# Kernel optimization log

Hardware: AMD Instinct MI355X
Metric: run time of the kernel (lower is better)

## Reference

```python
import jax, jax.numpy as jnp
import numpy as np

TOP_K = 4  # num_experts_per_tok


def setup_inputs() -> dict:
    key = jax.random.key(0)
    ks = jax.random.split(key, 5)
    T, H, M, E = 2048, 1024, 512, 32
    sH = 1.0 / np.sqrt(H)
    sM = 1.0 / np.sqrt(M)
    return {
        "x": jax.random.normal(ks[0], (T, 1, H), dtype=jnp.float32),
        "gate_w": jax.random.normal(ks[1], (E, H), dtype=jnp.float32) * sH,   # router nn.Linear weight [E, H]
        "w_gate": jax.random.normal(ks[2], (E, M, H), dtype=jnp.float32) * sH,  # ffn_gate_exps, per expert [M, H]
        "w_up": jax.random.normal(ks[3], (E, M, H), dtype=jnp.float32) * sH,    # ffn_up_exps
        "w_down": jax.random.normal(ks[4], (E, H, M), dtype=jnp.float32) * sM,  # ffn_down_exps, per expert [H, M]
    }


def reference(x, gate_w, w_gate, w_up, w_down):
    # x: [T, S, H]; only the last position is used (decode path)
    curr = x[:, -1, :]                                   # [T, H]
    T = curr.shape[0]
    E = gate_w.shape[0]

    # router: logits = curr @ gate_w^T, top-k, softmax over top-k logits
    logits = curr @ gate_w.T                             # [T, E]
    topk_vals, topk_ids = jax.lax.top_k(logits, TOP_K)   # [T, K]
    topk_weights = jax.nn.softmax(topk_vals, axis=-1)    # [T, K]

    # dense routing matrix [T, E]: weight for chosen experts, 0 elsewhere
    route = jnp.zeros((T, E), dtype=curr.dtype)
    route = route.at[jnp.arange(T)[:, None], topk_ids].add(topk_weights)

    # expert MLPs: gate/up -> silu(gate)*up -> down, weighted combine
    gate_act = jnp.einsum('th,emh->tem', curr, w_gate)   # [T, E, M]
    up_act = jnp.einsum('th,emh->tem', curr, w_up)
    mixed = jax.nn.silu(gate_act) * up_act * route[:, :, None]
    out = jnp.einsum('tem,ehm->th', mixed, w_down)       # [T, H]

    return out.reshape(T, 1, -1)
```

## Files before the change

kernel.cpp:

```cpp
#include <hip/hip_runtime.h>
#include <math.h>

#define T_TOK 2048
#define H_DIM 1024
#define M_DIM 512
#define E_NUM 32
#define TOPK  4

#define MAXT  63
#define SLOTS (MAXT * 256)

typedef __bf16 bf16x8 __attribute__((ext_vector_type(8)));
typedef float f32x4 __attribute__((ext_vector_type(4)));
typedef unsigned short u16x8 __attribute__((ext_vector_type(8)));
typedef unsigned short u16x4 __attribute__((ext_vector_type(4)));

__device__ __forceinline__ unsigned short f2bf(float f) {
  unsigned u = __float_as_uint(f);
  return (unsigned short)((u + 0x7fffu + ((u >> 16) & 1u)) >> 16);
}
__device__ __forceinline__ f32x4 mfma16(bf16x8 a, bf16x8 b, f32x4 c) {
  return __builtin_amdgcn_mfma_f32_16x16x32_bf16(a, b, c, 0, 0, 0);
}
__device__ __forceinline__ void gload16(const void* g, void* l) {
  __builtin_amdgcn_global_load_lds(
      (const __attribute__((address_space(1))) unsigned int*)g,
      (__attribute__((address_space(3))) unsigned int*)l, 16, 0, 0);
}

__global__ __launch_bounds__(256) void gating_kernel(
    const float* __restrict__ x, const float* __restrict__ gate_w,
    unsigned short* __restrict__ xh,
    float* __restrict__ topk_w, int* __restrict__ cursors,
    int* __restrict__ tok_list) {
  __shared__ float xr[H_DIM];
  __shared__ float logits[E_NUM];
  int t = blockIdx.x;
  int tid = threadIdx.x;
  const float* xrow = x + (size_t)t * H_DIM;
  float4 v = *(const float4*)(xrow + tid * 4);
  *(float4*)(xr + tid * 4) = v;
  {
    float f[4] = {v.x, v.y, v.z, v.w};
    u16x4 hv;
    #pragma unroll
    for (int j = 0; j < 4; ++j) hv[j] = f2bf(f[j]);
    *(u16x4*)(xh + (size_t)t * H_DIM + tid * 4) = hv;
  }
  __syncthreads();
  int wave = tid >> 6, lane = tid & 63;
  const float4* x4 = (const float4*)xr;
  for (int e8 = 0; e8 < 8; ++e8) {
    int e = wave * 8 + e8;
    const float4* g4 = (const float4*)(gate_w + (size_t)e * H_DIM);
    float p = 0.f;
    #pragma unroll
    for (int i = 0; i < 4; ++i) {
      float4 a = x4[lane + i * 64];
      float4 b = g4[lane + i * 64];
      p += a.x * b.x + a.y * b.y + a.z * b.z + a.w * b.w;
    }
    for (int off = 32; off > 0; off >>= 1) p += __shfl_down(p, off, 64);
    if (lane == 0) logits[e] = p;
  }
  __syncthreads();
  if (tid == 0) {
    float vv[E_NUM];
    for (int e = 0; e < E_NUM; ++e) vv[e] = logits[e];
    int ids[TOPK]; float vals[TOPK];
    for (int k = 0; k < TOPK; ++k) {
      int bi = 0; float bv = -1e30f;
      for (int e = 0; e < E_NUM; ++e) if (vv[e] > bv) { bv = vv[e]; bi = e; }
      ids[k] = bi; vals[k] = bv; vv[bi] = -1e30f;
    }
    float m = vals[0];
    float w[TOPK]; float s = 0.f;
    for (int k = 0; k < TOPK; ++k) { w[k] = expf(vals[k] - m); s += w[k]; }
    float inv = 1.f / s;
    for (int k = 0; k < TOPK; ++k) {
      int g = t * TOPK + k;
      topk_w[g] = w[k] * inv;
      int slot = atomicAdd(&cursors[ids[k]], 1);
      tok_list[ids[k] * T_TOK + slot] = g;
    }
  }
}

__global__ void build_tiles(const int* __restrict__ cursors,
                            int* __restrict__ n_tiles, int* __restrict__ tile_info) {
  int lane = threadIdx.x;
  int c = (lane < E_NUM) ? cursors[lane] : 0;
  int nt = (c + 255) >> 8;
  int pfx = nt;
  for (int off = 1; off < 64; off <<= 1) {
    int v = __shfl_up(pfx, off, 64);
    if (lane >= off) pfx += v;
  }
  if (lane == E_NUM - 1) n_tiles[0] = pfx;
  int excl = pfx - nt;
  if (lane < E_NUM)
    for (int i = 0; i < nt; ++i) tile_info[excl + i] = (lane << 8) | i;
}

__global__ __launch_bounds__(256) void fill_slots(
    const int* __restrict__ cursors, const int* __restrict__ n_tiles,
    const int* __restrict__ tile_info, const int* __restrict__ tok_list,
    int* __restrict__ slot_pair) {
  int b = blockIdx.x;
  int tid = threadIdx.x;
  int pair = -1;
  if (b < n_tiles[0]) {
    int info = tile_info[b];
    int e = info >> 8, i = info & 255;
    int idx = i * 256 + tid;
    if (idx < cursors[e]) pair = tok_list[e * T_TOK + idx];
  }
  slot_pair[b * 256 + tid] = pair;
}

template <int MODE>
__global__ __launch_bounds__(512, 2) void gemm256(
    const unsigned short* __restrict__ xh,
    const unsigned short* __restrict__ mixed,
    const float* __restrict__ w_gate, const float* __restrict__ w_up,
    const float* __restrict__ w_down,
    const int* __restrict__ n_tiles, const int* __restrict__ tile_info,
    const int* __restrict__ slot_pair,
    unsigned short* __restrict__ gu_raw, float* __restrict__ out) {
  constexpr int KT = (MODE == 0) ? H_DIM : M_DIM;
  constexpr int NKS = KT / 64;
  int tidx = blockIdx.y;
  if (tidx >= n_tiles[0]) return;
  int info = tile_info[tidx];
  int e = info >> 8;
  int n0 = blockIdx.x * 256;
  int slot0 = tidx * 256;
  int tid = threadIdx.x;
  int lane = tid & 63, wid = tid >> 6;

  __shared__ unsigned short L[2][32768];
  __shared__ int sp[256];

  if (tid < 256) sp[tid] = slot_pair[slot0 + tid];
  __syncthreads();

  const unsigned short* asrc[4];
  #pragma unroll
  for (int i = 0; i < 4; ++i) {
    int row = wid * 32 + i * 8 + (lane >> 3);
    int oct = (lane & 7) ^ (row & 7);
    if (MODE == 0) {
      int pr = sp[row];
      int tok = (pr >= 0) ? (pr >> 2) : 0;
      asrc[i] = xh + (size_t)tok * H_DIM + oct * 8;
    } else {
      asrc[i] = mixed + (size_t)(slot0 + row) * M_DIM + oct * 8;
    }
  }

  int brow = tid >> 1, bkh = (tid & 1) * 32;
  const float* bsrc;
  if (MODE == 0) {
    int n = n0 + brow;
    bsrc = (n < M_DIM ? w_gate + ((size_t)e * M_DIM + n) * H_DIM
                      : w_up + ((size_t)e * M_DIM + (n - M_DIM)) * H_DIM) + bkh;
  } else {
    bsrc = w_down + ((size_t)e * H_DIM + n0 + brow) * M_DIM + bkh;
  }
  int bwo[4];
  #pragma unroll
  for (int i = 0; i < 4; ++i)
    bwo[i] = 16384 + brow * 64 + ((((tid & 1) * 4 + i)) ^ (brow & 7)) * 8;

  int wm = wid >> 2, wn = wid & 3;
  f32x4 acc[8][4] = {};
  float fb[32];

#define G_LOADB(K0) { _Pragma("unroll") \
    for (int q = 0; q < 8; ++q) \
      *(float4*)(fb + q * 4) = *(const float4*)(bsrc + (K0) + q * 4); }

#define G_WRITEB(BB) { _Pragma("unroll") \
    for (int i = 0; i < 4; ++i) { \
      bf16x8 v; \
      _Pragma("unroll") \
      for (int j = 0; j < 8; ++j) v[j] = (__bf16)fb[i * 8 + j]; \
      *(bf16x8*)&L[BB][bwo[i]] = v; } }

#define G_DMA_A(BB, K0) { _Pragma("unroll") \
    for (int i = 0; i < 4; ++i) \
      gload16(asrc[i] + (K0), &L[BB][(wid * 32 + i * 8) * 64]); }

#define G_COMPUTE(BB) { _Pragma("unroll") \
    for (int kf = 0; kf < 2; ++kf) { \
      int kl = kf * 4 + (lane >> 4); \
      bf16x8 av[8], bv[4]; \
      _Pragma("unroll") \
      for (int mf = 0; mf < 8; ++mf) { \
        int ra = wm * 128 + mf * 16 + (lane & 15); \
        av[mf] = *(const bf16x8*)&L[BB][ra * 64 + (kl ^ (ra & 7)) * 8]; } \
      _Pragma("unroll") \
      for (int nf = 0; nf < 4; ++nf) { \
        int cb = wn * 64 + nf * 16 + (lane & 15); \
        bv[nf] = *(const bf16x8*)&L[BB][16384 + cb * 64 + (kl ^ (cb & 7)) * 8]; } \
      _Pragma("unroll") \
      for (int mf = 0; mf < 8; ++mf) \
        _Pragma("unroll") \
        for (int nf = 0; nf < 4; ++nf) \
          acc[mf][nf] = mfma16(av[mf], bv[nf], acc[mf][nf]); } }

  G_LOADB(0);
  G_DMA_A(0, 0);
  asm volatile("s_waitcnt vmcnt(0)" ::: "memory");
  __syncthreads();
  G_WRITEB(0);
  G_LOADB(64);

  for (int t = 0; t < NKS; ++t) {
    const int cur = t & 1;
    asm volatile("s_waitcnt vmcnt(0)" ::: "memory");
    __syncthreads();
    if (t + 1 < NKS) {
      G_WRITEB(cur ^ 1);
      G_DMA_A(cur ^ 1, (t + 1) * 64);
    }
    if (t + 2 < NKS) G_LOADB((t + 2) * 64);
    G_COMPUTE(cur);
  }

  if (MODE == 0) {
    #pragma unroll
    for (int mf = 0; mf < 8; ++mf)
      #pragma unroll
      for (int j = 0; j < 4; ++j) {
        int row = wm * 128 + mf * 16 + (lane >> 4) * 4 + j;
        size_t rb = (size_t)(slot0 + row) * 1024 + n0 + wn * 64 + (lane & 15);
        #pragma unroll
        for (int nf = 0; nf < 4; ++nf) {
          __bf16 v = (__bf16)acc[mf][nf][j];
          gu_raw[rb + nf * 16] = *(unsigned short*)&v;
        }
      }
  } else {
    #pragma unroll
    for (int mf = 0; mf < 8; ++mf)
      #pragma unroll
      for (int j = 0; j < 4; ++j) {
        int row = wm * 128 + mf * 16 + (lane >> 4) * 4 + j;
        int pr = sp[row];
        if (pr < 0) continue;
        size_t ob = (size_t)(pr >> 2) * H_DIM + n0 + wn * 64 + (lane & 15);
        #pragma unroll
        for (int nf = 0; nf < 4; ++nf)
          atomicAdd(&out[ob + nf * 16], acc[mf][nf][j]);
      }
  }
}

__global__ __launch_bounds__(256) void silu_kernel(
    const unsigned short* __restrict__ gu, const int* __restrict__ slot_pair,
    const float* __restrict__ topk_w, unsigned short* __restrict__ mixed) {
  int tid = threadIdx.x;
  int slot = blockIdx.x * 4 + (tid >> 6);
  int col = (tid & 63) * 8;
  int pr = slot_pair[slot];
  if (pr < 0) return;
  float w = topk_w[pr];
  const unsigned short* gp = gu + (size_t)slot * 1024 + col;
  u16x8 gg = *(const u16x8*)gp;
  u16x8 uu = *(const u16x8*)(gp + 512);
  bf16x8 o;
  #pragma unroll
  for (int j = 0; j < 8; ++j) {
    float g = __uint_as_float(((unsigned)gg[j]) << 16);
    float u = __uint_as_float(((unsigned)uu[j]) << 16);
    float v = (g / (1.f + __expf(-g))) * u * w;
    o[j] = (__bf16)v;
  }
  *(bf16x8*)(mixed + (size_t)slot * 512 + col) = o;
}

extern "C" void kernel_launch(void* const* d_in, const int* in_sizes, int n_in,
                              void* d_out, int out_size, void* d_ws, size_t ws_size,
                              hipStream_t stream) {
  const float* x      = (const float*)d_in[0];
  const float* gate_w = (const float*)d_in[1];
  const float* w_gate = (const float*)d_in[2];
  const float* w_up   = (const float*)d_in[3];
  const float* w_down = (const float*)d_in[4];
  float* out = (float*)d_out;

  char* ws = (char*)d_ws;
  size_t off = 0;
  float* topk_w    = (float*)(ws + off); off += (size_t)T_TOK * TOPK * 4;
  int*   cursors   = (int*)(ws + off);   off += 256;
  int*   n_tiles   = (int*)(ws + off);   off += 64;
  int*   tile_info = (int*)(ws + off);   off += MAXT * 4 + 64;
  int*   slot_pair = (int*)(ws + off);   off += (size_t)SLOTS * 4;
  int*   tok_list  = (int*)(ws + off);   off += (size_t)E_NUM * T_TOK * 4;
  unsigned short* x_hi   = (unsigned short*)(ws + off); off += (size_t)T_TOK * H_DIM * 2;
  unsigned short* gu_raw = (unsigned short*)(ws + off); off += (size_t)SLOTS * 1024 * 2;
  unsigned short* mixed  = (unsigned short*)(ws + off); off += (size_t)SLOTS * 512 * 2;

  hipMemsetAsync(cursors, 0, E_NUM * sizeof(int), stream);
  hipMemsetAsync(out, 0, (size_t)T_TOK * H_DIM * sizeof(float), stream);

  gating_kernel<<<T_TOK, 256, 0, stream>>>(x, gate_w, x_hi, topk_w,
                                           cursors, tok_list);
  build_tiles<<<1, 64, 0, stream>>>(cursors, n_tiles, tile_info);
  fill_slots<<<MAXT, 256, 0, stream>>>(cursors, n_tiles, tile_info, tok_list,
                                       slot_pair);
  gemm256<0><<<dim3(4, MAXT), 512, 0, stream>>>(
      x_hi, mixed, w_gate, w_up, w_down, n_tiles, tile_info, slot_pair,
      gu_raw, out);
  silu_kernel<<<SLOTS / 4, 256, 0, stream>>>(gu_raw, slot_pair, topk_w, mixed);
  gemm256<1><<<dim3(4, MAXT), 512, 0, stream>>>(
      x_hi, mixed, w_gate, w_up, w_down, n_tiles, tile_info, slot_pair,
      gu_raw, out);
}
```

Baseline: 201.0 us.

## Stream fp32 weights into LDS via direct DMA with triple-buffered K=32 pipeline

The grouped GEMM kernel no longer loads fp32 weight tiles into registers and converts them to bf16 before writing to LDS. Both A (bf16 activations) and B (raw fp32 weights) now go straight to LDS through global_load_lds, and the fp32-to-bf16 conversion happens at fragment read time. The K step drops from 64 to 32, and a three-stage ring buffer with counted vmcnt waits keeps two stages in flight. This aims to hide global latency and free registers, at the cost of more conversion ALU work per MFMA, twice the LDS bytes for B, and twice as many barriers per K.

```diff
diff --git a/kernel.cpp b/kernel.cpp
--- a/kernel.cpp
+++ b/kernel.cpp
@@ -26,6 +26,12 @@
   __builtin_amdgcn_global_load_lds(
       (const __attribute__((address_space(1))) unsigned int*)g,
       (__attribute__((address_space(3))) unsigned int*)l, 16, 0, 0);
+}
+__device__ __forceinline__ bf16x8 cvt8(f32x4 a, f32x4 b) {
+  bf16x8 r;
+  #pragma unroll
+  for (int j = 0; j < 4; ++j) { r[j] = (__bf16)a[j]; r[4 + j] = (__bf16)b[j]; }
+  return r;
 }
 
 __global__ __launch_bounds__(256) void gating_kernel(
@@ -128,7 +134,7 @@
     const int* __restrict__ slot_pair,
     unsigned short* __restrict__ gu_raw, float* __restrict__ out) {
   constexpr int KT = (MODE == 0) ? H_DIM : M_DIM;
-  constexpr int NKS = KT / 64;
+  constexpr int NKS = KT / 32;
   int tidx = blockIdx.y;
   if (tidx >= n_tiles[0]) return;
   int info = tile_info[tidx];
@@ -138,94 +144,102 @@
   int tid = threadIdx.x;
   int lane = tid & 63, wid = tid >> 6;
 
-  __shared__ unsigned short L[2][32768];
+  __shared__ unsigned short L[3][24576];
   __shared__ int sp[256];
 
   if (tid < 256) sp[tid] = slot_pair[slot0 + tid];
   __syncthreads();
 
-  const unsigned short* asrc[4];
-  #pragma unroll
-  for (int i = 0; i < 4; ++i) {
-    int row = wid * 32 + i * 8 + (lane >> 3);
-    int oct = (lane & 7) ^ (row & 7);
-    if (MODE == 0) {
-      int pr = sp[row];
-      int tok = (pr >= 0) ? (pr >> 2) : 0;
-      asrc[i] = xh + (size_t)tok * H_DIM + oct * 8;
+  const unsigned short* asrc0;
+  const unsigned short* asrc1;
+  {
+    #pragma unroll
+    for (int i = 0; i < 2; ++i) {
+      int blk = wid * 2 + i;
+      int row = blk * 16 + (lane >> 2);
+      int oct = ((lane & 3) - ((lane >> 2) >> 1)) & 3;
+      const unsigned short* s;
+      if (MODE == 0) {
+        int pr = sp[row];
+        int tok = (pr >= 0) ? (pr >> 2) : 0;
+        s = xh + (size_t)tok * H_DIM + oct * 8;
+      } else {
+        s = mixed + (size_t)(slot0 + row) * M_DIM + oct * 8;
+      }
+      if (i == 0) asrc0 = s; else asrc1 = s;
+    }
+  }
+  const float* bsrc0; const float* bsrc1; const float* bsrc2; const float* bsrc3;
+  {
+    #pragma unroll
+    for (int i = 0; i < 4; ++i) {
+      int ci = wid * 4 + i;
+      int blk = ci >> 1;
+      int w7 = ((ci & 1) << 6) + lane;
+      int col = blk * 16 + (w7 >> 3);
+      int q = ((w7 & 7) - ((w7 >> 3) & 7)) & 7;
+      const float* base;
+      if (MODE == 0) {
+        int n = n0 + col;
+        base = (n < M_DIM) ? w_gate + ((size_t)e * M_DIM + n) * H_DIM
+                           : w_up + ((size_t)e * M_DIM + (n - M_DIM)) * H_DIM;
+      } else {
+        base = w_down + ((size_t)e * H_DIM + n0 + col) * M_DIM;
+      }
+      base += q * 4;
+      if (i == 0) bsrc0 = base; else if (i == 1) bsrc1 = base;
+      else if (i == 2) bsrc2 = base; else bsrc3 = base;
+    }
+  }
+
+  int wm = wid >> 2, wn = wid & 3;
+  int l15 = lane & 15, o4 = lane >> 4, l7 = lane & 7;
+  f32x4 acc[8][4] = {};
+
+#define STAGE(P, KS) { \
+    gload16(asrc0 + (KS) * 32, &L[P][(wid * 2 + 0) * 512]); \
+    gload16(asrc1 + (KS) * 32, &L[P][(wid * 2 + 1) * 512]); \
+    gload16(bsrc0 + (KS) * 32, &L[P][8192 + (wid * 4 + 0) * 512]); \
+    gload16(bsrc1 + (KS) * 32, &L[P][8192 + (wid * 4 + 1) * 512]); \
+    gload16(bsrc2 + (KS) * 32, &L[P][8192 + (wid * 4 + 2) * 512]); \
+    gload16(bsrc3 + (KS) * 32, &L[P][8192 + (wid * 4 + 3) * 512]); }
+
+#define COMPUTE(P) { \
+    const unsigned short* Ab = &L[P][0]; \
+    const float* Bb = (const float*)&L[P][8192]; \
+    bf16x8 av[8]; bf16x8 bv[4]; \
+    _Pragma("unroll") \
+    for (int mf = 0; mf < 8; ++mf) { \
+      int idx = (wm * 8 + mf) * 512 + l15 * 32 + ((o4 + (l15 >> 1)) & 3) * 8; \
+      av[mf] = *(const bf16x8*)&Ab[idx]; } \
+    _Pragma("unroll") \
+    for (int nf = 0; nf < 4; ++nf) { \
+      int b0 = (wn * 4 + nf) * 512 + l15 * 32 + ((2 * o4 + l7) & 7) * 4; \
+      int b1 = (wn * 4 + nf) * 512 + l15 * 32 + ((2 * o4 + 1 + l7) & 7) * 4; \
+      bv[nf] = cvt8(*(const f32x4*)&Bb[b0], *(const f32x4*)&Bb[b1]); } \
+    _Pragma("unroll") \
+    for (int mf = 0; mf < 8; ++mf) \
+      _Pragma("unroll") \
+      for (int nf = 0; nf < 4; ++nf) \
+        acc[mf][nf] = mfma16(av[mf], bv[nf], acc[mf][nf]); }
+
+  STAGE(0, 0);
+  STAGE(1, 1);
+  for (int t = 0; t < NKS; ++t) {
+    int p = t % 3;
+    if (t + 2 < NKS) {
+      STAGE((t + 2) % 3, t + 2);
+      asm volatile("s_waitcnt vmcnt(12)" ::: "memory");
+    } else if (t + 1 < NKS) {
+      asm volatile("s_waitcnt vmcnt(6)" ::: "memory");
     } else {
-      asrc[i] = mixed + (size_t)(slot0 + row) * M_DIM + oct * 8;
-    }
-  }
-
-  int brow = tid >> 1, bkh = (tid & 1) * 32;
-  const float* bsrc;
-  if (MODE == 0) {
-    int n = n0 + brow;
-    bsrc = (n < M_DIM ? w_gate + ((size_t)e * M_DIM + n) * H_DIM
-                      : w_up + ((size_t)e * M_DIM + (n - M_DIM)) * H_DIM) + bkh;
-  } else {
-    bsrc = w_down + ((size_t)e * H_DIM + n0 + brow) * M_DIM + bkh;
-  }
-  int bwo[4];
-  #pragma unroll
-  for (int i = 0; i < 4; ++i)
-    bwo[i] = 16384 + brow * 64 + ((((tid & 1) * 4 + i)) ^ (brow & 7)) * 8;
-
-  int wm = wid >> 2, wn = wid & 3;
-  f32x4 acc[8][4] = {};
-  float fb[32];
-
-#define G_LOADB(K0) { _Pragma("unroll") \
-    for (int q = 0; q < 8; ++q) \
-      *(float4*)(fb + q * 4) = *(const float4*)(bsrc + (K0) + q * 4); }
-
-#define G_WRITEB(BB) { _Pragma("unroll") \
-    for (int i = 0; i < 4; ++i) { \
-      bf16x8 v; \
-      _Pragma("unroll") \
-      for (int j = 0; j < 8; ++j) v[j] = (__bf16)fb[i * 8 + j]; \
-      *(bf16x8*)&L[BB][bwo[i]] = v; } }
-
-#define G_DMA_A(BB, K0) { _Pragma("unroll") \
-    for (int i = 0; i < 4; ++i) \
-      gload16(asrc[i] + (K0), &L[BB][(wid * 32 + i * 8) * 64]); }
-
-#define G_COMPUTE(BB) { _Pragma("unroll") \
-    for (int kf = 0; kf < 2; ++kf) { \
-      int kl = kf * 4 + (lane >> 4); \
-      bf16x8 av[8], bv[4]; \
-      _Pragma("unroll") \
-      for (int mf = 0; mf < 8; ++mf) { \
-        int ra = wm * 128 + mf * 16 + (lane & 15); \
-        av[mf] = *(const bf16x8*)&L[BB][ra * 64 + (kl ^ (ra & 7)) * 8]; } \
-      _Pragma("unroll") \
-      for (int nf = 0; nf < 4; ++nf) { \
-        int cb = wn * 64 + nf * 16 + (lane & 15); \
-        bv[nf] = *(const bf16x8*)&L[BB][16384 + cb * 64 + (kl ^ (cb & 7)) * 8]; } \
-      _Pragma("unroll") \
-      for (int mf = 0; mf < 8; ++mf) \
-        _Pragma("unroll") \
-        for (int nf = 0; nf < 4; ++nf) \
-          acc[mf][nf] = mfma16(av[mf], bv[nf], acc[mf][nf]); } }
-
-  G_LOADB(0);
-  G_DMA_A(0, 0);
-  asm volatile("s_waitcnt vmcnt(0)" ::: "memory");
-  __syncthreads();
-  G_WRITEB(0);
-  G_LOADB(64);
-
-  for (int t = 0; t < NKS; ++t) {
-    const int cur = t & 1;
-    asm volatile("s_waitcnt vmcnt(0)" ::: "memory");
-    __syncthreads();
-    if (t + 1 < NKS) {
-      G_WRITEB(cur ^ 1);
-      G_DMA_A(cur ^ 1, (t + 1) * 64);
-    }
-    if (t + 2 < NKS) G_LOADB((t + 2) * 64);
-    G_COMPUTE(cur);
+      asm volatile("s_waitcnt vmcnt(0)" ::: "memory");
+    }
+    __builtin_amdgcn_s_barrier();
+    __builtin_amdgcn_sched_barrier(0);
+    COMPUTE(p);
+    asm volatile("s_waitcnt lgkmcnt(0)" ::: "memory");
+    __builtin_amdgcn_s_barrier();
   }
 
   if (MODE == 0) {
```

After: 199.1 us. Within noise of the previous version (-0.9%).
